# Performance work log

Hardware: AMD Instinct MI355X
Metric: run time of the kernel (lower is better)

## Reference

```python
import jax, jax.numpy as jnp
import numpy as np

N, E, D_IN, HID = 100000, 3200000, 256, 128
EPS = 1e-5  # BatchNorm1d default eps


def batchnorm(x, gamma, beta):
    # training-mode BatchNorm1d: batch stats, biased variance
    mu = x.mean(axis=0)
    var = ((x - mu) ** 2).mean(axis=0)
    return (x - mu) * jax.lax.rsqrt(var + EPS) * gamma + beta


def setup_inputs() -> dict:
    key = jax.random.key(0)
    ks = jax.random.split(key, 6)
    s_in = 1.0 / np.sqrt(D_IN)
    s_h = 1.0 / np.sqrt(HID)
    return {
        "x": jax.random.normal(ks[0], (N, D_IN), jnp.float32),
        "edge_index": jax.random.randint(ks[1], (2, E), 0, N),
        "W1": jax.random.uniform(ks[2], (D_IN, HID), jnp.float32, -s_in, s_in),
        "b1": jnp.zeros((HID,), jnp.float32),
        "g1": jnp.ones((HID,), jnp.float32),
        "be1": jnp.zeros((HID,), jnp.float32),
        "Wl": jax.random.uniform(ks[3], (HID, HID), jnp.float32, -s_h, s_h),
        "bl": jnp.zeros((HID,), jnp.float32),
        "Wr": jax.random.uniform(ks[4], (HID, HID), jnp.float32, -s_h, s_h),
        "g2": jnp.ones((HID,), jnp.float32),
        "be2": jnp.zeros((HID,), jnp.float32),
    }


def reference(x, edge_index, W1, b1, g1, be1, Wl, bl, Wr, g2, be2):
    # input_linear: Linear -> BatchNorm1d, then ReLU
    feat = jax.nn.relu(batchnorm(x @ W1 + b1, g1, be1))  # [N, HID]

    # SAGEConv: mean-aggregate source features at destinations
    src, dst = edge_index[0], edge_index[1]
    msg_sum = jax.ops.segment_sum(feat[src], dst, num_segments=N)       # [N, HID]
    deg = jax.ops.segment_sum(jnp.ones((E, 1), feat.dtype), dst, num_segments=N)
    mean = msg_sum / jnp.maximum(deg, 1.0)

    # out = lin_l(aggr) + lin_r(x); lin_l has bias, lin_r does not (PyG default)
    out = mean @ Wl + bl + feat @ Wr
    out_feat = batchnorm(out, g2, be2)
    return feat, out_feat
```

## Files before the change

### kernel.cpp

```cpp
#include <hip/hip_runtime.h>

#define NN 100000
#define NE 3200000
#define KD 256
#define HD 128
#define NB 782
#define CAP 4608

typedef __bf16 bf16x8 __attribute__((ext_vector_type(8)));
typedef float  f32x8  __attribute__((ext_vector_type(8)));
typedef float  f32x4  __attribute__((ext_vector_type(4)));
typedef float  f32x2  __attribute__((ext_vector_type(2)));
typedef unsigned u32x2 __attribute__((ext_vector_type(2)));
typedef unsigned u32x4 __attribute__((ext_vector_type(4)));

__device__ __forceinline__ f32x4 mfma16(bf16x8 a, bf16x8 b, f32x4 c) {
  return __builtin_amdgcn_mfma_f32_16x16x32_bf16(a, b, c, 0, 0, 0);
}

__global__ void prep_w(const float* __restrict__ W1, const float* __restrict__ Wl,
                       const float* __restrict__ Wr, __bf16* __restrict__ Bt1,
                       __bf16* __restrict__ Bt2, float* __restrict__ stats,
                       int* __restrict__ bucket_cur) {
  if (blockIdx.x == 0) {
    for (int i = threadIdx.x; i < 1024; i += 256) stats[i] = 0.f;
  } else if (blockIdx.x == 1) {
    for (int i = threadIdx.x; i < NB; i += 256) bucket_cur[i] = i * CAP;
  }
  int c = blockIdx.x;
  int k = threadIdx.x;
  Bt1[c * KD + k] = (__bf16)W1[k * HD + c];
  float w = (k < HD) ? Wl[k * HD + c] : Wr[(k - HD) * HD + c];
  Bt2[c * KD + k] = (__bf16)w;
}

__global__ __launch_bounds__(1024) void b_scatter(const int* __restrict__ src,
                                                  const int* __restrict__ dst,
                                                  int* __restrict__ bucket_cur,
                                                  unsigned* __restrict__ pairs) {
  __shared__ int h[NB];
  __shared__ int cur[NB];
  __shared__ int gbase[NB];
  for (int i = threadIdx.x; i < NB; i += 1024) { h[i] = 0; cur[i] = 0; }
  __syncthreads();
  int base = blockIdx.x * 12500;
  for (int i = threadIdx.x; i < 12500; i += 1024)
    atomicAdd(&h[dst[base + i] >> 7], 1);
  __syncthreads();
  for (int b = threadIdx.x; b < NB; b += 1024) {
    int c = h[b];
    gbase[b] = c ? atomicAdd(&bucket_cur[b], c) : 0;
  }
  __syncthreads();
  for (int i = threadIdx.x; i < 12500; i += 1024) {
    int d = dst[base + i];
    int s = src[base + i];
    int b = d >> 7;
    int r = atomicAdd(&cur[b], 1);
    pairs[gbase[b] + r] = ((unsigned)s << 7) | (unsigned)(d & 127);
  }
}

__global__ __launch_bounds__(256) void b_sort(const int* __restrict__ bucket_cur,
                                              unsigned* __restrict__ pc,
                                              int* __restrict__ row_start,
                                              int* __restrict__ row_cnt) {
  __shared__ unsigned sin[CAP];
  __shared__ unsigned sout[CAP];
  __shared__ int h[128], ex[128];
  int b = blockIdx.x;
  int n0 = b * CAP;
  int cnt = bucket_cur[b] - n0;
  if (cnt > CAP) cnt = CAP;
  if (threadIdx.x < 128) h[threadIdx.x] = 0;
  __syncthreads();
  for (int i = threadIdx.x; i < cnt; i += 256) {
    unsigned v = pc[n0 + i];
    sin[i] = v;
    atomicAdd(&h[v & 127], 1);
  }
  __syncthreads();
  if (threadIdx.x < 128) ex[threadIdx.x] = h[threadIdx.x];
  __syncthreads();
  for (int off = 1; off < 128; off <<= 1) {
    int u = 0;
    if (threadIdx.x < 128 && threadIdx.x >= off) u = ex[threadIdx.x - off];
    __syncthreads();
    if (threadIdx.x < 128) ex[threadIdx.x] += u;
    __syncthreads();
  }
  if (threadIdx.x < 128) {
    int c = h[threadIdx.x];
    int excl = ex[threadIdx.x] - c;
    int node = b * 128 + threadIdx.x;
    if (node < NN) {
      row_start[node] = n0 + excl;
      row_cnt[node] = c;
    }
    h[threadIdx.x] = excl;
  }
  __syncthreads();
  for (int i = threadIdx.x; i < cnt; i += 256) {
    unsigned v = sin[i];
    int r = atomicAdd(&h[v & 127], 1);
    sout[r] = v >> 7;
  }
  __syncthreads();
  for (int i = threadIdx.x; i < cnt; i += 256)
    pc[n0 + i] = sout[i];
}

__global__ __launch_bounds__(256, 2) void gemm_x(const float* __restrict__ A,
                                                 const __bf16* __restrict__ Bt,
                                                 float* __restrict__ C,
                                                 float* __restrict__ sumc,
                                                 float* __restrict__ sqc) {
  __shared__ __bf16 sB[HD * KD];
  __shared__ float lsum[HD], lsq[HD];
  int tid = threadIdx.x;
  if (tid < HD) { lsum[tid] = 0.f; lsq[tid] = 0.f; }
  int wave = tid >> 6, lane = tid & 63;
  int q = lane >> 4, m = lane & 15;
  int rowbase = blockIdx.x * 256 + wave * 64;
  for (int i = tid; i < HD * KD / 8; i += 256) {
    int r = i >> 5, g = i & 31;
    bf16x8 v = *(const bf16x8*)(Bt + (size_t)r * KD + (g << 3));
    *(bf16x8*)(&sB[r * KD + ((g ^ (r & 7)) << 3)]) = v;
  }
  bf16x8 areg[4][8];
#pragma unroll
  for (int g = 0; g < 4; ++g) {
    int r = rowbase + g * 16 + m;
    if (r > NN - 1) r = NN - 1;
    const float* pa = A + (size_t)r * KD + q * 8;
    f32x8 u[8];
#pragma unroll
    for (int k = 0; k < 8; ++k) u[k] = *(const f32x8*)(pa + k * 32);
#pragma unroll
    for (int k = 0; k < 8; ++k) areg[g][k] = __builtin_convertvector(u[k], bf16x8);
  }
  __syncthreads();
#pragma unroll
  for (int hh = 0; hh < 2; ++hh) {
    f32x4 acc[4][4];
    f32x4 z = {0.f, 0.f, 0.f, 0.f};
#pragma unroll
    for (int g = 0; g < 4; ++g)
#pragma unroll
      for (int t = 0; t < 4; ++t) acc[g][t] = z;
#pragma unroll
    for (int ks = 0; ks < 8; ++ks) {
      int gb = ks * 4 + q;
#pragma unroll
      for (int t = 0; t < 4; ++t) {
        int c = hh * 64 + t * 16 + m;
        bf16x8 bb = *(const bf16x8*)(&sB[c * KD + ((gb ^ (c & 7)) << 3)]);
#pragma unroll
        for (int g = 0; g < 4; ++g) acc[g][t] = mfma16(areg[g][ks], bb, acc[g][t]);
      }
    }
    float ps[4], pq2[4];
#pragma unroll
    for (int t = 0; t < 4; ++t) { ps[t] = 0.f; pq2[t] = 0.f; }
#pragma unroll
    for (int g = 0; g < 4; ++g)
#pragma unroll
      for (int rg = 0; rg < 4; ++rg) {
        int r = rowbase + g * 16 + q * 4 + rg;
        if (r < NN) {
          float* Cr = C + (size_t)r * HD + hh * 64 + m;
#pragma unroll
          for (int t = 0; t < 4; ++t) {
            float v = acc[g][t][rg];
            Cr[t * 16] = v;
            ps[t] += v;
            pq2[t] += v * v;
          }
        }
      }
#pragma unroll
    for (int t = 0; t < 4; ++t) {
      atomicAdd(&lsum[hh * 64 + t * 16 + m], ps[t]);
      atomicAdd(&lsq[hh * 64 + t * 16 + m], pq2[t]);
    }
  }
  __syncthreads();
  if (tid < HD) {
    atomicAdd(&sumc[tid], lsum[tid]);
    atomicAdd(&sqc[tid], lsq[tid]);
  }
}

__global__ __launch_bounds__(256, 2) void gemm_cat(const __bf16* __restrict__ A0,
                                                   const __bf16* __restrict__ A1,
                                                   const __bf16* __restrict__ Bt,
                                                   float* __restrict__ C,
                                                   float* __restrict__ sumc,
                                                   float* __restrict__ sqc) {
  __shared__ __bf16 sB[HD * KD];
  __shared__ float lsum[HD], lsq[HD];
  int tid = threadIdx.x;
  if (tid < HD) { lsum[tid] = 0.f; lsq[tid] = 0.f; }
  int wave = tid >> 6, lane = tid & 63;
  int q = lane >> 4, m = lane & 15;
  int rowbase = blockIdx.x * 256 + wave * 64;
  for (int i = tid; i < HD * KD / 8; i += 256) {
    int r = i >> 5, g = i & 31;
    bf16x8 v = *(const bf16x8*)(Bt + (size_t)r * KD + (g << 3));
    *(bf16x8*)(&sB[r * KD + ((g ^ (r & 7)) << 3)]) = v;
  }
  bf16x8 areg[4][8];
#pragma unroll
  for (int g = 0; g < 4; ++g) {
    int r = rowbase + g * 16 + m;
    if (r > NN - 1) r = NN - 1;
    const __bf16* p0 = A0 + (size_t)r * HD + q * 8;
    const __bf16* p1 = A1 + (size_t)r * HD + q * 8;
#pragma unroll
    for (int k = 0; k < 4; ++k) areg[g][k] = *(const bf16x8*)(p0 + k * 32);
#pragma unroll
    for (int k = 0; k < 4; ++k) areg[g][4 + k] = *(const bf16x8*)(p1 + k * 32);
  }
  __syncthreads();
#pragma unroll
  for (int hh = 0; hh < 2; ++hh) {
    f32x4 acc[4][4];
    f32x4 z = {0.f, 0.f, 0.f, 0.f};
#pragma unroll
    for (int g = 0; g < 4; ++g)
#pragma unroll
      for (int t = 0; t < 4; ++t) acc[g][t] = z;
#pragma unroll
    for (int ks = 0; ks < 8; ++ks) {
      int gb = ks * 4 + q;
#pragma unroll
      for (int t = 0; t < 4; ++t) {
        int c = hh * 64 + t * 16 + m;
        bf16x8 bb = *(const bf16x8*)(&sB[c * KD + ((gb ^ (c & 7)) << 3)]);
#pragma unroll
        for (int g = 0; g < 4; ++g) acc[g][t] = mfma16(areg[g][ks], bb, acc[g][t]);
      }
    }
    float ps[4], pq2[4];
#pragma unroll
    for (int t = 0; t < 4; ++t) { ps[t] = 0.f; pq2[t] = 0.f; }
#pragma unroll
    for (int g = 0; g < 4; ++g)
#pragma unroll
      for (int rg = 0; rg < 4; ++rg) {
        int r = rowbase + g * 16 + q * 4 + rg;
        if (r < NN) {
          float* Cr = C + (size_t)r * HD + hh * 64 + m;
#pragma unroll
          for (int t = 0; t < 4; ++t) {
            float v = acc[g][t][rg];
            Cr[t * 16] = v;
            ps[t] += v;
            pq2[t] += v * v;
          }
        }
      }
#pragma unroll
    for (int t = 0; t < 4; ++t) {
      atomicAdd(&lsum[hh * 64 + t * 16 + m], ps[t]);
      atomicAdd(&lsq[hh * 64 + t * 16 + m], pq2[t]);
    }
  }
  __syncthreads();
  if (tid < HD) {
    atomicAdd(&sumc[tid], lsum[tid]);
    atomicAdd(&sqc[tid], lsq[tid]);
  }
}

__global__ __launch_bounds__(256) void bn_apply(const float* __restrict__ X,
                                                const float* __restrict__ sumc,
                                                const float* __restrict__ sqc,
                                                const float* __restrict__ g,
                                                const float* __restrict__ be,
                                                float* __restrict__ outf,
                                                __bf16* __restrict__ outb,
                                                unsigned char* __restrict__ outq,
                                                int relu) {
  __shared__ float sc[HD], sh[HD];
  if (threadIdx.x < HD) {
    int c = threadIdx.x;
    float mu = sumc[c] * (1.0f / NN);
    float var = sqc[c] * (1.0f / NN) - mu * mu;
    float rs = rsqrtf(var + 1e-5f);
    float a = rs * g[c];
    sc[c] = a;
    sh[c] = be[c] - mu * a;
  }
  __syncthreads();
  size_t base = ((size_t)blockIdx.x * 256 + threadIdx.x) * 8;
  int c0 = (int)(base & (HD - 1));
  f32x4 x0 = *(const f32x4*)(X + base);
  f32x4 x1 = *(const f32x4*)(X + base + 4);
  float o[8];
#pragma unroll
  for (int j = 0; j < 8; ++j) {
    float xv = (j < 4) ? x0[j] : x1[j - 4];
    float v = xv * sc[c0 + j] + sh[c0 + j];
    if (relu) v = fmaxf(v, 0.f);
    o[j] = v;
  }
  f32x4 o0 = {o[0], o[1], o[2], o[3]};
  f32x4 o1 = {o[4], o[5], o[6], o[7]};
  *(f32x4*)(outf + base) = o0;
  *(f32x4*)(outf + base + 4) = o1;
  if (outb) {
    bf16x8 ob;
#pragma unroll
    for (int j = 0; j < 8; ++j) ob[j] = (__bf16)o[j];
    *(bf16x8*)(outb + base) = ob;
    int w0 = 0, w1 = 0;
    w0 = __builtin_amdgcn_cvt_pk_fp8_f32(o[0], o[1], w0, false);
    w0 = __builtin_amdgcn_cvt_pk_fp8_f32(o[2], o[3], w0, true);
    w1 = __builtin_amdgcn_cvt_pk_fp8_f32(o[4], o[5], w1, false);
    w1 = __builtin_amdgcn_cvt_pk_fp8_f32(o[6], o[7], w1, true);
    u32x2 qv = {(unsigned)w0, (unsigned)w1};
    *(u32x2*)(outq + base) = qv;
  }
}

__global__ __launch_bounds__(256) void aggregate(const int* __restrict__ row_start,
                                                 const int* __restrict__ row_cnt,
                                                 const unsigned* __restrict__ csr,
                                                 const unsigned char* __restrict__ featq,
                                                 __bf16* __restrict__ meanb) {
  int node = blockIdx.x * 4 + (threadIdx.x >> 6);
  if (node >= NN) return;
  int lane = threadIdx.x & 63;
  int sub = lane >> 3;
  int m = lane & 7;
  unsigned moff = (unsigned)m * 16u;
  int s = row_start[node];
  int deg = row_cnt[node];
  int e = s + deg;
  f32x2 acc[8];
#pragma unroll
  for (int j = 0; j < 8; ++j) acc[j] = (f32x2){0.f, 0.f};

#define ACC8(v)                                                        \
  do {                                                                 \
    acc[0] += __builtin_amdgcn_cvt_pk_f32_fp8((int)(v).x, false);      \
    acc[1] += __builtin_amdgcn_cvt_pk_f32_fp8((int)(v).x, true);       \
    acc[2] += __builtin_amdgcn_cvt_pk_f32_fp8((int)(v).y, false);      \
    acc[3] += __builtin_amdgcn_cvt_pk_f32_fp8((int)(v).y, true);       \
    acc[4] += __builtin_amdgcn_cvt_pk_f32_fp8((int)(v).z, false);      \
    acc[5] += __builtin_amdgcn_cvt_pk_f32_fp8((int)(v).z, true);       \
    acc[6] += __builtin_amdgcn_cvt_pk_f32_fp8((int)(v).w, false);      \
    acc[7] += __builtin_amdgcn_cvt_pk_f32_fp8((int)(v).w, true);       \
  } while (0)

  for (int base = s; base < e; base += 64) {
    int nb = e - base;
    if (nb > 64) nb = 64;
    unsigned my = (lane < nb) ? csr[base + lane] : 0u;
    {
      unsigned sn0 = __shfl(my, sub, 64);
      unsigned sn1 = __shfl(my, sub + 8, 64);
      unsigned sn2 = __shfl(my, sub + 16, 64);
      unsigned sn3 = __shfl(my, sub + 24, 64);
      bool a0 = sub < nb, a1 = sub + 8 < nb, a2 = sub + 16 < nb, a3 = sub + 24 < nb;
      u32x4 v0 = *(const u32x4*)(featq + (((a0 ? sn0 : 0u) << 7) + moff));
      u32x4 v1 = *(const u32x4*)(featq + (((a1 ? sn1 : 0u) << 7) + moff));
      u32x4 v2 = *(const u32x4*)(featq + (((a2 ? sn2 : 0u) << 7) + moff));
      u32x4 v3 = *(const u32x4*)(featq + (((a3 ? sn3 : 0u) << 7) + moff));
      if (a0) ACC8(v0);
      if (a1) ACC8(v1);
      if (a2) ACC8(v2);
      if (a3) ACC8(v3);
    }
    if (nb > 32) {
      unsigned sn0 = __shfl(my, sub + 32, 64);
      unsigned sn1 = __shfl(my, sub + 40, 64);
      unsigned sn2 = __shfl(my, sub + 48, 64);
      unsigned sn3 = __shfl(my, sub + 56, 64);
      bool a0 = sub + 32 < nb, a1 = sub + 40 < nb, a2 = sub + 48 < nb, a3 = sub + 56 < nb;
      u32x4 v0 = *(const u32x4*)(featq + (((a0 ? sn0 : 0u) << 7) + moff));
      u32x4 v1 = *(const u32x4*)(featq + (((a1 ? sn1 : 0u) << 7) + moff));
      u32x4 v2 = *(const u32x4*)(featq + (((a2 ? sn2 : 0u) << 7) + moff));
      u32x4 v3 = *(const u32x4*)(featq + (((a3 ? sn3 : 0u) << 7) + moff));
      if (a0) ACC8(v0);
      if (a1) ACC8(v1);
      if (a2) ACC8(v2);
      if (a3) ACC8(v3);
    }
  }
#undef ACC8

#pragma unroll
  for (int j = 0; j < 8; ++j) {
    acc[j].x += __shfl_xor(acc[j].x, 8, 64);
    acc[j].y += __shfl_xor(acc[j].y, 8, 64);
    acc[j].x += __shfl_xor(acc[j].x, 16, 64);
    acc[j].y += __shfl_xor(acc[j].y, 16, 64);
    acc[j].x += __shfl_xor(acc[j].x, 32, 64);
    acc[j].y += __shfl_xor(acc[j].y, 32, 64);
  }
  if (sub == 0) {
    float inv = 1.0f / (float)(deg < 1 ? 1 : deg);
    bf16x8 o0, o1;
#pragma unroll
    for (int j = 0; j < 4; ++j) {
      o0[2 * j]     = (__bf16)(acc[j].x * inv);
      o0[2 * j + 1] = (__bf16)(acc[j].y * inv);
      o1[2 * j]     = (__bf16)(acc[4 + j].x * inv);
      o1[2 * j + 1] = (__bf16)(acc[4 + j].y * inv);
    }
    __bf16* dst = meanb + (size_t)node * HD + m * 16;
    *(bf16x8*)dst = o0;
    *(bf16x8*)(dst + 8) = o1;
  }
}

extern "C" void kernel_launch(void* const* d_in, const int* in_sizes, int n_in,
                              void* d_out, int out_size, void* d_ws, size_t ws_size,
                              hipStream_t stream) {
  (void)in_sizes; (void)n_in; (void)out_size; (void)ws_size;
  const float* x   = (const float*)d_in[0];
  const int*   ei  = (const int*)d_in[1];
  const float* W1  = (const float*)d_in[2];
  const float* g1  = (const float*)d_in[4];
  const float* be1 = (const float*)d_in[5];
  const float* Wl  = (const float*)d_in[6];
  const float* Wr  = (const float*)d_in[8];
  const float* g2  = (const float*)d_in[9];
  const float* be2 = (const float*)d_in[10];

  float* feat_out = (float*)d_out;
  float* out_feat = feat_out + (size_t)NN * HD;
  unsigned char* featq = (unsigned char*)out_feat;

  char* w = (char*)d_ws;
  float*    h          = (float*)(w);
  __bf16*   featb      = (__bf16*)(w + 51200000);
  __bf16*   meanb      = (__bf16*)(w + 76800000);
  unsigned* pc         = (unsigned*)(w + 102400000);
  int*      row_start  = (int*)(w + 116814848);
  int*      row_cnt    = (int*)(w + 117214848);
  int*      bucket_cur = (int*)(w + 117614848);
  float*    stats      = (float*)(w + 117618944);
  __bf16*   Bt1        = (__bf16*)(w + 117623040);
  __bf16*   Bt2        = (__bf16*)(w + 117688576);

  float* sum1 = stats,       * sq1 = stats + 128;
  float* sum2 = stats + 512, * sq2 = stats + 640;

  const int* esrc = ei;
  const int* edst = ei + NE;

  prep_w<<<128, 256, 0, stream>>>(W1, Wl, Wr, Bt1, Bt2, stats, bucket_cur);
  b_scatter<<<256, 1024, 0, stream>>>(esrc, edst, bucket_cur, pc);
  b_sort<<<NB, 256, 0, stream>>>(bucket_cur, pc, row_start, row_cnt);

  gemm_x<<<391, 256, 0, stream>>>(x, Bt1, h, sum1, sq1);
  bn_apply<<<6250, 256, 0, stream>>>(h, sum1, sq1, g1, be1, feat_out, featb, featq, 1);

  aggregate<<<25000, 256, 0, stream>>>(row_start, row_cnt, pc, featq, meanb);

  gemm_cat<<<391, 256, 0, stream>>>(meanb, featb, Bt2, h, sum2, sq2);
  bn_apply<<<6250, 256, 0, stream>>>(h, sum2, sq2, g2, be2, out_feat,
                                     (__bf16*)nullptr, (unsigned char*)nullptr, 0);
}
```

Baseline: 430.1 us.

## Halve GEMM row tile, split weight staging over K, raise occupancy

Result: slower. 470.6 us (+9.4%).

```diff
diff --git a/kernel.cpp b/kernel.cpp
--- a/kernel.cpp
+++ b/kernel.cpp
@@ -110,79 +110,96 @@
     pc[n0 + i] = sout[i];
 }
 
-__global__ __launch_bounds__(256, 2) void gemm_x(const float* __restrict__ A,
+__global__ __launch_bounds__(256, 3) void gemm_x(const float* __restrict__ A,
                                                  const __bf16* __restrict__ Bt,
                                                  float* __restrict__ C,
                                                  float* __restrict__ sumc,
                                                  float* __restrict__ sqc) {
-  __shared__ __bf16 sB[HD * KD];
+  __shared__ __bf16 sB[HD * 128];
   __shared__ float lsum[HD], lsq[HD];
   int tid = threadIdx.x;
   if (tid < HD) { lsum[tid] = 0.f; lsq[tid] = 0.f; }
   int wave = tid >> 6, lane = tid & 63;
   int q = lane >> 4, m = lane & 15;
-  int rowbase = blockIdx.x * 256 + wave * 64;
-  for (int i = tid; i < HD * KD / 8; i += 256) {
-    int r = i >> 5, g = i & 31;
-    bf16x8 v = *(const bf16x8*)(Bt + (size_t)r * KD + (g << 3));
-    *(bf16x8*)(&sB[r * KD + ((g ^ (r & 7)) << 3)]) = v;
-  }
-  bf16x8 areg[4][8];
-#pragma unroll
-  for (int g = 0; g < 4; ++g) {
+  int rowbase = blockIdx.x * 128 + wave * 32;
+  f32x8 u[2][8];
+#pragma unroll
+  for (int g = 0; g < 2; ++g) {
     int r = rowbase + g * 16 + m;
     if (r > NN - 1) r = NN - 1;
     const float* pa = A + (size_t)r * KD + q * 8;
-    f32x8 u[8];
-#pragma unroll
-    for (int k = 0; k < 8; ++k) u[k] = *(const f32x8*)(pa + k * 32);
-#pragma unroll
-    for (int k = 0; k < 8; ++k) areg[g][k] = __builtin_convertvector(u[k], bf16x8);
-  }
-  __syncthreads();
-#pragma unroll
-  for (int hh = 0; hh < 2; ++hh) {
-    f32x4 acc[4][4];
-    f32x4 z = {0.f, 0.f, 0.f, 0.f};
-#pragma unroll
-    for (int g = 0; g < 4; ++g)
-#pragma unroll
-      for (int t = 0; t < 4; ++t) acc[g][t] = z;
-#pragma unroll
-    for (int ks = 0; ks < 8; ++ks) {
-      int gb = ks * 4 + q;
-#pragma unroll
-      for (int t = 0; t < 4; ++t) {
-        int c = hh * 64 + t * 16 + m;
-        bf16x8 bb = *(const bf16x8*)(&sB[c * KD + ((gb ^ (c & 7)) << 3)]);
-#pragma unroll
-        for (int g = 0; g < 4; ++g) acc[g][t] = mfma16(areg[g][ks], bb, acc[g][t]);
-      }
-    }
-    float ps[4], pq2[4];
-#pragma unroll
-    for (int t = 0; t < 4; ++t) { ps[t] = 0.f; pq2[t] = 0.f; }
-#pragma unroll
-    for (int g = 0; g < 4; ++g)
-#pragma unroll
-      for (int rg = 0; rg < 4; ++rg) {
-        int r = rowbase + g * 16 + q * 4 + rg;
-        if (r < NN) {
-          float* Cr = C + (size_t)r * HD + hh * 64 + m;
-#pragma unroll
-          for (int t = 0; t < 4; ++t) {
-            float v = acc[g][t][rg];
-            Cr[t * 16] = v;
-            ps[t] += v;
-            pq2[t] += v * v;
-          }
+#pragma unroll
+    for (int k = 0; k < 8; ++k) u[g][k] = *(const f32x8*)(pa + k * 32);
+  }
+  for (int i = tid; i < 128 * 16; i += 256) {
+    int r = i >> 4, g = i & 15;
+    bf16x8 v = *(const bf16x8*)(Bt + (size_t)r * KD + (g << 3));
+    *(bf16x8*)(&sB[r * 128 + ((g ^ (r & 7)) << 3)]) = v;
+  }
+  bf16x8 areg[2][8];
+#pragma unroll
+  for (int g = 0; g < 2; ++g)
+#pragma unroll
+    for (int k = 0; k < 8; ++k) areg[g][k] = __builtin_convertvector(u[g][k], bf16x8);
+  f32x4 acc[2][8];
+  f32x4 z = {0.f, 0.f, 0.f, 0.f};
+#pragma unroll
+  for (int g = 0; g < 2; ++g)
+#pragma unroll
+    for (int t = 0; t < 8; ++t) acc[g][t] = z;
+  __syncthreads();
+#pragma unroll
+  for (int ks = 0; ks < 4; ++ks) {
+    int gb = ks * 4 + q;
+#pragma unroll
+    for (int t = 0; t < 8; ++t) {
+      int c = t * 16 + m;
+      bf16x8 bb = *(const bf16x8*)(&sB[c * 128 + ((gb ^ (c & 7)) << 3)]);
+      acc[0][t] = mfma16(areg[0][ks], bb, acc[0][t]);
+      acc[1][t] = mfma16(areg[1][ks], bb, acc[1][t]);
+    }
+  }
+  __syncthreads();
+  for (int i = tid; i < 128 * 16; i += 256) {
+    int r = i >> 4, g = i & 15;
+    bf16x8 v = *(const bf16x8*)(Bt + (size_t)r * KD + 128 + (g << 3));
+    *(bf16x8*)(&sB[r * 128 + ((g ^ (r & 7)) << 3)]) = v;
+  }
+  __syncthreads();
+#pragma unroll
+  for (int ks = 0; ks < 4; ++ks) {
+    int gb = ks * 4 + q;
+#pragma unroll
+    for (int t = 0; t < 8; ++t) {
+      int c = t * 16 + m;
+      bf16x8 bb = *(const bf16x8*)(&sB[c * 128 + ((gb ^ (c & 7)) << 3)]);
+      acc[0][t] = mfma16(areg[0][4 + ks], bb, acc[0][t]);
+      acc[1][t] = mfma16(areg[1][4 + ks], bb, acc[1][t]);
+    }
+  }
+  float ps[8], pq2[8];
+#pragma unroll
+  for (int t = 0; t < 8; ++t) { ps[t] = 0.f; pq2[t] = 0.f; }
+#pragma unroll
+  for (int g = 0; g < 2; ++g)
+#pragma unroll
+    for (int rg = 0; rg < 4; ++rg) {
+      int r = rowbase + g * 16 + q * 4 + rg;
+      if (r < NN) {
+        float* Cr = C + (size_t)r * HD + m;
+#pragma unroll
+        for (int t = 0; t < 8; ++t) {
+          float v = acc[g][t][rg];
+          Cr[t * 16] = v;
+          ps[t] += v;
+          pq2[t] += v * v;
         }
       }
-#pragma unroll
-    for (int t = 0; t < 4; ++t) {
-      atomicAdd(&lsum[hh * 64 + t * 16 + m], ps[t]);
-      atomicAdd(&lsq[hh * 64 + t * 16 + m], pq2[t]);
-    }
+    }
+#pragma unroll
+  for (int t = 0; t < 8; ++t) {
+    atomicAdd(&lsum[t * 16 + m], ps[t]);
+    atomicAdd(&lsq[t * 16 + m], pq2[t]);
   }
   __syncthreads();
   if (tid < HD) {
@@ -191,27 +208,22 @@
   }
 }
 
-__global__ __launch_bounds__(256, 2) void gemm_cat(const __bf16* __restrict__ A0,
+__global__ __launch_bounds__(256, 3) void gemm_cat(const __bf16* __restrict__ A0,
                                                    const __bf16* __restrict__ A1,
                                                    const __bf16* __restrict__ Bt,
                                                    float* __restrict__ C,
                                                    float* __restrict__ sumc,
                                                    float* __restrict__ sqc) {
-  __shared__ __bf16 sB[HD * KD];
+  __shared__ __bf16 sB[HD * 128];
   __shared__ float lsum[HD], lsq[HD];
   int tid = threadIdx.x;
   if (tid < HD) { lsum[tid] = 0.f; lsq[tid] = 0.f; }
   int wave = tid >> 6, lane = tid & 63;
   int q = lane >> 4, m = lane & 15;
-  int rowbase = blockIdx.x * 256 + wave * 64;
-  for (int i = tid; i < HD * KD / 8; i += 256) {
-    int r = i >> 5, g = i & 31;
-    bf16x8 v = *(const bf16x8*)(Bt + (size_t)r * KD + (g << 3));
-    *(bf16x8*)(&sB[r * KD + ((g ^ (r & 7)) << 3)]) = v;
-  }
-  bf16x8 areg[4][8];
-#pragma unroll
-  for (int g = 0; g < 4; ++g) {
+  int rowbase = blockIdx.x * 128 + wave * 32;
+  bf16x8 areg[2][8];
+#pragma unroll
+  for (int g = 0; g < 2; ++g) {
     int r = rowbase + g * 16 + m;
     if (r > NN - 1) r = NN - 1;
     const __bf16* p0 = A0 + (size_t)r * HD + q * 8;
@@ -221,50 +233,70 @@
 #pragma unroll
     for (int k = 0; k < 4; ++k) areg[g][4 + k] = *(const bf16x8*)(p1 + k * 32);
   }
-  __syncthreads();
-#pragma unroll
-  for (int hh = 0; hh < 2; ++hh) {
-    f32x4 acc[4][4];
-    f32x4 z = {0.f, 0.f, 0.f, 0.f};
-#pragma unroll
-    for (int g = 0; g < 4; ++g)
-#pragma unroll
-      for (int t = 0; t < 4; ++t) acc[g][t] = z;
-#pragma unroll
-    for (int ks = 0; ks < 8; ++ks) {
-      int gb = ks * 4 + q;
-#pragma unroll
-      for (int t = 0; t < 4; ++t) {
-        int c = hh * 64 + t * 16 + m;
-        bf16x8 bb = *(const bf16x8*)(&sB[c * KD + ((gb ^ (c & 7)) << 3)]);
-#pragma unroll
-        for (int g = 0; g < 4; ++g) acc[g][t] = mfma16(areg[g][ks], bb, acc[g][t]);
-      }
-    }
-    float ps[4], pq2[4];
-#pragma unroll
-    for (int t = 0; t < 4; ++t) { ps[t] = 0.f; pq2[t] = 0.f; }
-#pragma unroll
-    for (int g = 0; g < 4; ++g)
-#pragma unroll
-      for (int rg = 0; rg < 4; ++rg) {
-        int r = rowbase + g * 16 + q * 4 + rg;
-        if (r < NN) {
-          float* Cr = C + (size_t)r * HD + hh * 64 + m;
-#pragma unroll
-          for (int t = 0; t < 4; ++t) {
-            float v = acc[g][t][rg];
-            Cr[t * 16] = v;
-            ps[t] += v;
-            pq2[t] += v * v;
-          }
+  for (int i = tid; i < 128 * 16; i += 256) {
+    int r = i >> 4, g = i & 15;
+    bf16x8 v = *(const bf16x8*)(Bt + (size_t)r * KD + (g << 3));
+    *(bf16x8*)(&sB[r * 128 + ((g ^ (r & 7)) << 3)]) = v;
+  }
+  f32x4 acc[2][8];
+  f32x4 z = {0.f, 0.f, 0.f, 0.f};
+#pragma unroll
+  for (int g = 0; g < 2; ++g)
+#pragma unroll
+    for (int t = 0; t < 8; ++t) acc[g][t] = z;
+  __syncthreads();
+#pragma unroll
+  for (int ks = 0; ks < 4; ++ks) {
+    int gb = ks * 4 + q;
+#pragma unroll
+    for (int t = 0; t < 8; ++t) {
+      int c = t * 16 + m;
+      bf16x8 bb = *(const bf16x8*)(&sB[c * 128 + ((gb ^ (c & 7)) << 3)]);
+      acc[0][t] = mfma16(areg[0][ks], bb, acc[0][t]);
+      acc[1][t] = mfma16(areg[1][ks], bb, acc[1][t]);
+    }
+  }
+  __syncthreads();
+  for (int i = tid; i < 128 * 16; i += 256) {
+    int r = i >> 4, g = i & 15;
+    bf16x8 v = *(const bf16x8*)(Bt + (size_t)r * KD + 128 + (g << 3));
+    *(bf16x8*)(&sB[r * 128 + ((g ^ (r & 7)) << 3)]) = v;
+  }
+  __syncthreads();
+#pragma unroll
+  for (int ks = 0; ks < 4; ++ks) {
+    int gb = ks * 4 + q;
+#pragma unroll
+    for (int t = 0; t < 8; ++t) {
+      int c = t * 16 + m;
+      bf16x8 bb = *(const bf16x8*)(&sB[c * 128 + ((gb ^ (c & 7)) << 3)]);
+      acc[0][t] = mfma16(areg[0][4 + ks], bb, acc[0][t]);
+      acc[1][t] = mfma16(areg[1][4 + ks], bb, acc[1][t]);
+    }
+  }
+  float ps[8], pq2[8];
+#pragma unroll
+  for (int t = 0; t < 8; ++t) { ps[t] = 0.f; pq2[t] = 0.f; }
+#pragma unroll
+  for (int g = 0; g < 2; ++g)
+#pragma unroll
+    for (int rg = 0; rg < 4; ++rg) {
+      int r = rowbase + g * 16 + q * 4 + rg;
+      if (r < NN) {
+        float* Cr = C + (size_t)r * HD + m;
+#pragma unroll
+        for (int t = 0; t < 8; ++t) {
+          float v = acc[g][t][rg];
+          Cr[t * 16] = v;
+          ps[t] += v;
+          pq2[t] += v * v;
         }
       }
-#pragma unroll
-    for (int t = 0; t < 4; ++t) {
-      atomicAdd(&lsum[hh * 64 + t * 16 + m], ps[t]);
-      atomicAdd(&lsq[hh * 64 + t * 16 + m], pq2[t]);
-    }
+    }
+#pragma unroll
+  for (int t = 0; t < 8; ++t) {
+    atomicAdd(&lsum[t * 16 + m], ps[t]);
+    atomicAdd(&lsq[t * 16 + m], pq2[t]);
   }
   __syncthreads();
   if (tid < HD) {
@@ -456,12 +488,12 @@
   b_scatter<<<256, 1024, 0, stream>>>(esrc, edst, bucket_cur, pc);
   b_sort<<<NB, 256, 0, stream>>>(bucket_cur, pc, row_start, row_cnt);
 
-  gemm_x<<<391, 256, 0, stream>>>(x, Bt1, h, sum1, sq1);
+  gemm_x<<<782, 256, 0, stream>>>(x, Bt1, h, sum1, sq1);
   bn_apply<<<6250, 256, 0, stream>>>(h, sum1, sq1, g1, be1, feat_out, featb, featq, 1);
 
   aggregate<<<25000, 256, 0, stream>>>(row_start, row_cnt, pc, featq, meanb);
 
-  gemm_cat<<<391, 256, 0, stream>>>(meanb, featb, Bt2, h, sum2, sq2);
+  gemm_cat<<<782, 256, 0, stream>>>(meanb, featb, Bt2, h, sum2, sq2);
   bn_apply<<<6250, 256, 0, stream>>>(h, sum2, sq2, g2, be2, out_feat,
                                      (__bf16*)nullptr, (unsigned char*)nullptr, 0);
 }
```
